# Optimization experiments

Hardware: AMD Instinct MI355X
Metric: run time of the kernel (lower is better)

Reference implementation:

```python
import jax, jax.numpy as jnp
import numpy as np

B, S, D, H, C = 2, 2048, 1024, 16, 64

def setup_inputs() -> dict:
    key = jax.random.key(0)
    kx, kq, kk, kv, ko = jax.random.split(key, 5)
    scale = 0.02
    return {
        "x": jax.random.normal(kx, (B, S, D), dtype=jnp.float32),
        "Wq": jax.random.normal(kq, (D, H, C), dtype=jnp.float32) * scale,
        "Wk": jax.random.normal(kk, (D, H, C), dtype=jnp.float32) * scale,
        "Wv": jax.random.normal(kv, (D, H, C), dtype=jnp.float32) * scale,
        "Wo": jax.random.normal(ko, (H, C, D), dtype=jnp.float32) * scale,
    }

def reference(x, Wq, Wk, Wv, Wo):
    # project to per-head q/k/v: [B,S,H,C]
    q = jnp.einsum('bqd,dhc->bqhc', x, Wq)
    k = jnp.einsum('bkd,dhc->bkhc', x, Wk)
    v = jnp.einsum('bkd,dhc->bkhc', x, Wv)
    q = q * (C ** -0.5)
    alphas = jnp.einsum('bqhc,bkhc->bhqk', q, k)  # [B,H,S,S]
    weights = jax.nn.softmax(alphas, axis=-1)
    out = jnp.einsum('bhqk,bkhc->bqhc', weights, v)
    return jnp.einsum('bqhc,hcd->bqd', out, Wo)
```

## Files before the change

### kernel.cpp

```cpp
#include <hip/hip_runtime.h>
#include <hip/hip_bf16.h>
#include <stdint.h>
#include <stddef.h>

typedef __bf16 bf16;
typedef __bf16 bf16x8 __attribute__((ext_vector_type(8)));
typedef float f32x4 __attribute__((ext_vector_type(4)));

#define DEV __device__ __forceinline__

DEV void async16(const bf16* g, bf16* l) {
    __builtin_amdgcn_global_load_lds(
        (const __attribute__((address_space(1))) void*)g,
        (__attribute__((address_space(3))) void*)l,
        16, 0, 0);
}


__global__ void convert_x(const float* __restrict__ in, bf16* __restrict__ out, int n) {
    int i = (blockIdx.x * blockDim.x + threadIdx.x) * 4;
    if (i >= n) return;
    const float4 v = *(const float4*)(in + i);
    bf16 o4[4] = {(bf16)v.x, (bf16)v.y, (bf16)v.z, (bf16)v.w};
    *(uint2*)(out + i) = *(const uint2*)o4;
}

__global__ void transpose_cvt_all(const float* __restrict__ Wq, const float* __restrict__ Wk,
                                  const float* __restrict__ Wv, const float* __restrict__ Wo,
                                  bf16* __restrict__ WqkvT, bf16* __restrict__ WoT) {
    const float* src;
    bf16* dst;
    float scale = 1.0f;
    switch (blockIdx.z) {
        case 0: src = Wq; dst = WqkvT; scale = 0.125f * 1.4426950408889634f; break;
        case 1: src = Wk; dst = WqkvT + 1024 * 1024; break;
        case 2: src = Wv; dst = WqkvT + 2 * 1024 * 1024; break;
        default: src = Wo; dst = WoT; break;
    }
    __shared__ float t[32][33];
    const int c0 = blockIdx.x * 32, r0 = blockIdx.y * 32;
    const int tx = threadIdx.x & 31, ty = threadIdx.x >> 5;
#pragma unroll
    for (int i = 0; i < 32; i += 8)
        t[ty + i][tx] = src[(size_t)(r0 + ty + i) * 1024 + c0 + tx];
    __syncthreads();
#pragma unroll
    for (int i = 0; i < 32; i += 8)
        dst[(size_t)(c0 + ty + i) * 1024 + r0 + tx] = (bf16)(t[tx][ty + i] * scale);
}

__global__ void transpose_v(const bf16* __restrict__ V, bf16* __restrict__ VT) {
    __shared__ bf16 t[32][33];
    const int c0 = blockIdx.x * 32, r0 = blockIdx.y * 32;
    const int tx = threadIdx.x & 31, ty = threadIdx.x >> 5;
#pragma unroll
    for (int i = 0; i < 32; i += 8)
        t[ty + i][tx] = V[(size_t)(r0 + ty + i) * 3072 + c0 + tx];
    __syncthreads();
#pragma unroll
    for (int i = 0; i < 32; i += 8)
        VT[(size_t)(c0 + ty + i) * 4096 + r0 + tx] = t[tx][ty + i];
}


template <bool OUT_F32>
__global__ __launch_bounds__(256, 3) void gemm_bt(
    const bf16* __restrict__ A, const bf16* __restrict__ BT, void* __restrict__ Cout,
    int M, int N, int K) {
    __shared__ __attribute__((aligned(16))) bf16 As[2 * 128 * 32];
    __shared__ __attribute__((aligned(16))) bf16 Bs[2 * 128 * 32];
    const int tid = threadIdx.x;
    const int wid = tid >> 6;
    const int lane = tid & 63;
    const int quad = lane >> 4;
    const int l16 = lane & 15;
    const int wm = wid >> 1, wn = wid & 1;
    const int m0 = blockIdx.y * 128, n0 = blockIdx.x * 128;

    const int srow = wid * 32 + (lane >> 2);
    const int skcol = (lane & 3) * 8;
    const bf16* ag = A + (size_t)(m0 + srow) * K + skcol;
    const bf16* bg = BT + (size_t)(n0 + srow) * K + skcol;

    f32x4 acc[4][4];
#pragma unroll
    for (int i = 0; i < 4; ++i)
#pragma unroll
        for (int j = 0; j < 4; ++j) acc[i][j] = (f32x4){0.f, 0.f, 0.f, 0.f};

    for (int k0 = 0; k0 < K; k0 += 64) {
#pragma unroll
        for (int p = 0; p < 2; ++p) {
            async16(ag + k0 + p * 32, &As[p * 4096 + (wid * 32) * 32]);
            async16(ag + (size_t)16 * K + k0 + p * 32, &As[p * 4096 + (wid * 32 + 16) * 32]);
            async16(bg + k0 + p * 32, &Bs[p * 4096 + (wid * 32) * 32]);
            async16(bg + (size_t)16 * K + k0 + p * 32, &Bs[p * 4096 + (wid * 32 + 16) * 32]);
        }
        __syncthreads();

#pragma unroll
        for (int ks = 0; ks < 2; ++ks) {
            bf16x8 af[4], bfr[4];
#pragma unroll
            for (int mi = 0; mi < 4; ++mi)
                af[mi] = *(const bf16x8*)&As[ks * 4096 + (wm * 64 + mi * 16 + l16) * 32 + quad * 8];
#pragma unroll
            for (int ni = 0; ni < 4; ++ni)
                bfr[ni] = *(const bf16x8*)&Bs[ks * 4096 + (wn * 64 + ni * 16 + l16) * 32 + quad * 8];
#pragma unroll
            for (int mi = 0; mi < 4; ++mi)
#pragma unroll
                for (int ni = 0; ni < 4; ++ni)
                    acc[mi][ni] = __builtin_amdgcn_mfma_f32_16x16x32_bf16(
                        af[mi], bfr[ni], acc[mi][ni], 0, 0, 0);
        }
        __syncthreads();
    }

    if (OUT_F32) {
        float* C = (float*)Cout;
#pragma unroll
        for (int mi = 0; mi < 4; ++mi)
#pragma unroll
            for (int ni = 0; ni < 4; ++ni)
#pragma unroll
                for (int r = 0; r < 4; ++r)
                    C[(size_t)(m0 + wm * 64 + mi * 16 + quad * 4 + r) * N +
                      (n0 + wn * 64 + ni * 16 + l16)] = acc[mi][ni][r];
    } else {
        bf16* C = (bf16*)Cout;
#pragma unroll
        for (int mi = 0; mi < 4; ++mi)
#pragma unroll
            for (int ni = 0; ni < 4; ++ni)
#pragma unroll
                for (int r = 0; r < 4; ++r)
                    C[(size_t)(m0 + wm * 64 + mi * 16 + quad * 4 + r) * N +
                      (n0 + wn * 64 + ni * 16 + l16)] = (bf16)acc[mi][ni][r];
    }
}


__global__ __launch_bounds__(256, 4) void flash_attn(
    const bf16* __restrict__ QKV, const bf16* __restrict__ VT,
    float* __restrict__ op, float* __restrict__ lp) {
    constexpr int LDK = 72;
    constexpr int LDP = 68;
    __shared__ __attribute__((aligned(16))) bf16 Ks[64 * LDK];
    __shared__ __attribute__((aligned(16))) bf16 Vs[64 * LDK];
    __shared__ __attribute__((aligned(16))) bf16 Ps[128 * LDP];

    const int tid = threadIdx.x, wid = tid >> 6, lane = tid & 63;
    const int quad = lane >> 4, l16 = lane & 15;
    const int qt = blockIdx.x;
    const int bh = blockIdx.y;
    const int kh = blockIdx.z;
    const int b = bh >> 4, h = bh & 15;
    const int q0 = qt * 128;

    const int row8 = tid >> 3, col8 = (tid & 7) * 8;

    {
        const bf16* qg = QKV + (size_t)(b * 2048 + q0 + row8) * 3072 + h * 64 + col8;
#pragma unroll
        for (int p = 0; p < 4; ++p)
            *(bf16x8*)&Ps[(p * 32 + row8) * LDP + col8] =
                *(const bf16x8*)(qg + (size_t)(p * 32) * 3072);
    }
    __syncthreads();
    bf16x8 qf[2][2];
#pragma unroll
    for (int mi = 0; mi < 2; ++mi)
#pragma unroll
        for (int ks = 0; ks < 2; ++ks)
            qf[mi][ks] = *(const bf16x8*)&Ps[(wid * 32 + mi * 16 + l16) * LDP + ks * 32 + quad * 8];

    const bf16* kg = QKV + (size_t)(b * 2048 + kh * 1024 + row8) * 3072 + 1024 + h * 64 + col8;
    const bf16* vg = VT + (size_t)(h * 64 + row8) * 4096 + b * 2048 + kh * 1024 + col8;

    bf16x8 kr0 = *(const bf16x8*)(kg);
    bf16x8 kr1 = *(const bf16x8*)(kg + (size_t)32 * 3072);
    bf16x8 vr0 = *(const bf16x8*)(vg);
    bf16x8 vr1 = *(const bf16x8*)(vg + (size_t)32 * 4096);

    f32x4 o[2][4];
    float lsum[2][4];
#pragma unroll
    for (int mi = 0; mi < 2; ++mi) {
#pragma unroll
        for (int ni = 0; ni < 4; ++ni) o[mi][ni] = (f32x4){0.f, 0.f, 0.f, 0.f};
#pragma unroll
        for (int r = 0; r < 4; ++r) lsum[mi][r] = 0.f;
    }

    for (int kc = 0; kc < 16; ++kc) {
        *(bf16x8*)&Ks[row8 * LDK + col8] = kr0;
        *(bf16x8*)&Ks[(row8 + 32) * LDK + col8] = kr1;
        *(bf16x8*)&Vs[row8 * LDK + col8] = vr0;
        *(bf16x8*)&Vs[(row8 + 32) * LDK + col8] = vr1;
        __syncthreads();

        if (kc < 15) {
            const size_t ko = (size_t)(kc + 1) * 64;
            kr0 = *(const bf16x8*)(kg + ko * 3072);
            kr1 = *(const bf16x8*)(kg + (ko + 32) * 3072);
            vr0 = *(const bf16x8*)(vg + ko);
            vr1 = *(const bf16x8*)(vg + (size_t)32 * 4096 + ko);
        }

        f32x4 s[2][4];
#pragma unroll
        for (int mi = 0; mi < 2; ++mi)
#pragma unroll
            for (int ni = 0; ni < 4; ++ni) s[mi][ni] = (f32x4){0.f, 0.f, 0.f, 0.f};
#pragma unroll
        for (int ni = 0; ni < 4; ++ni) {
            const bf16x8 kf0 = *(const bf16x8*)&Ks[(ni * 16 + l16) * LDK + quad * 8];
            const bf16x8 kf1 = *(const bf16x8*)&Ks[(ni * 16 + l16) * LDK + 32 + quad * 8];
#pragma unroll
            for (int mi = 0; mi < 2; ++mi) {
                s[mi][ni] = __builtin_amdgcn_mfma_f32_16x16x32_bf16(qf[mi][0], kf0, s[mi][ni], 0, 0, 0);
                s[mi][ni] = __builtin_amdgcn_mfma_f32_16x16x32_bf16(qf[mi][1], kf1, s[mi][ni], 0, 0, 0);
            }
        }

#pragma unroll
        for (int mi = 0; mi < 2; ++mi)
#pragma unroll
            for (int ni = 0; ni < 4; ++ni)
#pragma unroll
                for (int r = 0; r < 4; ++r) {
                    const float p = __builtin_amdgcn_exp2f(s[mi][ni][r]);
                    lsum[mi][r] += p;
                    Ps[(wid * 32 + mi * 16 + quad * 4 + r) * LDP + ni * 16 + l16] = (bf16)p;
                }

#pragma unroll
        for (int ks = 0; ks < 2; ++ks) {
            bf16x8 pf[2];
#pragma unroll
            for (int mi = 0; mi < 2; ++mi)
                pf[mi] = *(const bf16x8*)&Ps[(wid * 32 + mi * 16 + l16) * LDP + ks * 32 + quad * 8];
#pragma unroll
            for (int ni = 0; ni < 4; ++ni) {
                const bf16x8 vf = *(const bf16x8*)&Vs[(ni * 16 + l16) * LDK + ks * 32 + quad * 8];
#pragma unroll
                for (int mi = 0; mi < 2; ++mi)
                    o[mi][ni] = __builtin_amdgcn_mfma_f32_16x16x32_bf16(pf[mi], vf, o[mi][ni], 0, 0, 0);
            }
        }
        __syncthreads();
    }

#pragma unroll
    for (int off = 1; off < 16; off <<= 1)
#pragma unroll
        for (int mi = 0; mi < 2; ++mi)
#pragma unroll
            for (int r = 0; r < 4; ++r) lsum[mi][r] += __shfl_xor(lsum[mi][r], off);

    if (l16 == 0) {
#pragma unroll
        for (int mi = 0; mi < 2; ++mi)
#pragma unroll
            for (int r = 0; r < 4; ++r)
                lp[(size_t)kh * 4096 * 16 +
                   (size_t)(b * 2048 + q0 + wid * 32 + mi * 16 + quad * 4 + r) * 16 + h] = lsum[mi][r];
    }
#pragma unroll
    for (int mi = 0; mi < 2; ++mi)
#pragma unroll
        for (int ni = 0; ni < 4; ++ni)
#pragma unroll
            for (int r = 0; r < 4; ++r)
                op[(size_t)kh * 4096 * 1024 +
                   (size_t)(b * 2048 + q0 + wid * 32 + mi * 16 + quad * 4 + r) * 1024 +
                   (h * 64 + ni * 16 + l16)] = o[mi][ni][r];
}

__global__ void combine_att(const float* __restrict__ op, const float* __restrict__ lp,
                            bf16* __restrict__ att) {
    const int idx = (blockIdx.x * 256 + threadIdx.x) * 4;
    const int q = idx >> 10, h = (idx & 1023) >> 6;
    const float4 a = *(const float4*)(op + idx);
    const float4 c = *(const float4*)(op + (size_t)4096 * 1024 + idx);
    const float l = lp[q * 16 + h] + lp[4096 * 16 + q * 16 + h];
    const float inv = 1.0f / l;
    bf16 r[4] = {(bf16)((a.x + c.x) * inv), (bf16)((a.y + c.y) * inv),
                 (bf16)((a.z + c.z) * inv), (bf16)((a.w + c.w) * inv)};
    *(uint2*)(att + idx) = *(const uint2*)r;
}


extern "C" void kernel_launch(void* const* d_in, const int* in_sizes, int n_in,
                              void* d_out, int out_size, void* d_ws, size_t ws_size,
                              hipStream_t stream) {
    (void)in_sizes; (void)n_in; (void)out_size; (void)ws_size;
    const float* x  = (const float*)d_in[0];
    const float* Wq = (const float*)d_in[1];
    const float* Wk = (const float*)d_in[2];
    const float* Wv = (const float*)d_in[3];
    const float* Wo = (const float*)d_in[4];

    char* ws = (char*)d_ws;
    bf16* xb    = (bf16*)(ws);
    bf16* att   = xb;
    bf16* WqkvT = (bf16*)(ws + (size_t)8  * 1024 * 1024);
    bf16* WoT   = (bf16*)(ws + (size_t)14 * 1024 * 1024);
    bf16* QKV   = (bf16*)(ws + (size_t)16 * 1024 * 1024);
    bf16* VT    = (bf16*)(ws + (size_t)40 * 1024 * 1024);
    float* op   = (float*)(ws + (size_t)48 * 1024 * 1024);
    float* lp   = (float*)(ws + (size_t)80 * 1024 * 1024);

    const int n_x = 2 * 2048 * 1024;
    convert_x<<<n_x / (256 * 4), 256, 0, stream>>>(x, xb, n_x);

    transpose_cvt_all<<<dim3(32, 32, 4), 256, 0, stream>>>(Wq, Wk, Wv, Wo, WqkvT, WoT);

    gemm_bt<false><<<dim3(3072 / 128, 4096 / 128), 256, 0, stream>>>(
        xb, WqkvT, QKV, 4096, 3072, 1024);

    transpose_v<<<dim3(32, 128), 256, 0, stream>>>(QKV + 2048, VT);

    flash_attn<<<dim3(16, 32, 2), 256, 0, stream>>>(QKV, VT, op, lp);

    combine_att<<<4096, 256, 0, stream>>>(op, lp, att);

    gemm_bt<true><<<dim3(1024 / 128, 4096 / 128), 256, 0, stream>>>(
        att, WoT, (float*)d_out, 4096, 1024, 1024);
}
```

Baseline: 205.0 us.

## Fuse attention normalization into flash kernel with in-register P and intra-block key split

The flash attention kernel is restructured. It computes S transposed so that the softmax probabilities stay in registers and feed the PV MFMA directly, zero-padding half of the MFMA K dimension. Keys are split across the four waves of a block and the partial outputs are reduced through LDS. This replaces the grid-level key split, the fp32 partial-output and denominator buffers, and the separate combine kernel. K and V are read straight from global memory without LDS staging. The costs are wasted MFMA work from the padding, heavy register pressure (launch bounds lowered to 2), and half as many blocks.

```diff
diff --git a/kernel.cpp b/kernel.cpp
--- a/kernel.cpp
+++ b/kernel.cpp
@@ -4,6 +4,7 @@
 #include <stddef.h>
 
 typedef __bf16 bf16;
+typedef __bf16 bf16x4 __attribute__((ext_vector_type(4)));
 typedef __bf16 bf16x8 __attribute__((ext_vector_type(8)));
 typedef float f32x4 __attribute__((ext_vector_type(4)));
 
@@ -141,154 +142,135 @@
 }
 
 
-__global__ __launch_bounds__(256, 4) void flash_attn(
-    const bf16* __restrict__ QKV, const bf16* __restrict__ VT,
-    float* __restrict__ op, float* __restrict__ lp) {
-    constexpr int LDK = 72;
-    constexpr int LDP = 68;
-    __shared__ __attribute__((aligned(16))) bf16 Ks[64 * LDK];
-    __shared__ __attribute__((aligned(16))) bf16 Vs[64 * LDK];
-    __shared__ __attribute__((aligned(16))) bf16 Ps[128 * LDP];
+__global__ __launch_bounds__(256, 2) void flash_attn(
+    const bf16* __restrict__ QKV, const bf16* __restrict__ VT, bf16* __restrict__ att) {
+    __shared__ float Osc[2][32 * 256];
+    __shared__ float Lred[4][128];
+    __shared__ float Linv[128];
 
     const int tid = threadIdx.x, wid = tid >> 6, lane = tid & 63;
     const int quad = lane >> 4, l16 = lane & 15;
     const int qt = blockIdx.x;
     const int bh = blockIdx.y;
-    const int kh = blockIdx.z;
     const int b = bh >> 4, h = bh & 15;
     const int q0 = qt * 128;
 
-    const int row8 = tid >> 3, col8 = (tid & 7) * 8;
-
+    bf16x8 qf[8][2];
     {
-        const bf16* qg = QKV + (size_t)(b * 2048 + q0 + row8) * 3072 + h * 64 + col8;
-#pragma unroll
-        for (int p = 0; p < 4; ++p)
-            *(bf16x8*)&Ps[(p * 32 + row8) * LDP + col8] =
-                *(const bf16x8*)(qg + (size_t)(p * 32) * 3072);
-    }
-    __syncthreads();
-    bf16x8 qf[2][2];
-#pragma unroll
-    for (int mi = 0; mi < 2; ++mi)
-#pragma unroll
-        for (int ks = 0; ks < 2; ++ks)
-            qf[mi][ks] = *(const bf16x8*)&Ps[(wid * 32 + mi * 16 + l16) * LDP + ks * 32 + quad * 8];
-
-    const bf16* kg = QKV + (size_t)(b * 2048 + kh * 1024 + row8) * 3072 + 1024 + h * 64 + col8;
-    const bf16* vg = VT + (size_t)(h * 64 + row8) * 4096 + b * 2048 + kh * 1024 + col8;
-
-    bf16x8 kr0 = *(const bf16x8*)(kg);
-    bf16x8 kr1 = *(const bf16x8*)(kg + (size_t)32 * 3072);
-    bf16x8 vr0 = *(const bf16x8*)(vg);
-    bf16x8 vr1 = *(const bf16x8*)(vg + (size_t)32 * 4096);
-
-    f32x4 o[2][4];
-    float lsum[2][4];
-#pragma unroll
-    for (int mi = 0; mi < 2; ++mi) {
-#pragma unroll
-        for (int ni = 0; ni < 4; ++ni) o[mi][ni] = (f32x4){0.f, 0.f, 0.f, 0.f};
-#pragma unroll
-        for (int r = 0; r < 4; ++r) lsum[mi][r] = 0.f;
-    }
-
-    for (int kc = 0; kc < 16; ++kc) {
-        *(bf16x8*)&Ks[row8 * LDK + col8] = kr0;
-        *(bf16x8*)&Ks[(row8 + 32) * LDK + col8] = kr1;
-        *(bf16x8*)&Vs[row8 * LDK + col8] = vr0;
-        *(bf16x8*)&Vs[(row8 + 32) * LDK + col8] = vr1;
-        __syncthreads();
-
-        if (kc < 15) {
-            const size_t ko = (size_t)(kc + 1) * 64;
-            kr0 = *(const bf16x8*)(kg + ko * 3072);
-            kr1 = *(const bf16x8*)(kg + (ko + 32) * 3072);
-            vr0 = *(const bf16x8*)(vg + ko);
-            vr1 = *(const bf16x8*)(vg + (size_t)32 * 4096 + ko);
+        const bf16* qbase = QKV + (size_t)(b * 2048 + q0 + l16) * 3072 + h * 64 + quad * 8;
+#pragma unroll
+        for (int mi = 0; mi < 8; ++mi)
+#pragma unroll
+            for (int ks = 0; ks < 2; ++ks)
+                qf[mi][ks] = *(const bf16x8*)(qbase + (size_t)mi * 16 * 3072 + ks * 32);
+    }
+
+    const bf16* kbase = QKV + (size_t)(b * 2048 + wid * 16 + l16) * 3072 + 1024 + h * 64 + quad * 8;
+    const bf16* vbase = VT + (size_t)(h * 64 + l16) * 4096 + b * 2048 + wid * 16 + quad * 4;
+
+    f32x4 o[8][4];
+#pragma unroll
+    for (int mi = 0; mi < 8; ++mi)
+#pragma unroll
+        for (int ct = 0; ct < 4; ++ct) o[mi][ct] = (f32x4){0.f, 0.f, 0.f, 0.f};
+    float lsum[8];
+#pragma unroll
+    for (int mi = 0; mi < 8; ++mi) lsum[mi] = 0.f;
+
+    for (int kc = 0; kc < 32; ++kc) {
+        const bf16* kp = kbase + (size_t)kc * 64 * 3072;
+        const bf16x8 kf0 = *(const bf16x8*)(kp);
+        const bf16x8 kf1 = *(const bf16x8*)(kp + 32);
+
+        const bf16* vp = vbase + kc * 64;
+        bf16x8 vf[4];
+#pragma unroll
+        for (int ct = 0; ct < 4; ++ct) {
+            const bf16x4 t = *(const bf16x4*)(vp + (size_t)ct * 16 * 4096);
+            vf[ct] = (bf16x8){t[0], t[1], t[2], t[3],
+                              (bf16)0.f, (bf16)0.f, (bf16)0.f, (bf16)0.f};
         }
 
-        f32x4 s[2][4];
-#pragma unroll
-        for (int mi = 0; mi < 2; ++mi)
-#pragma unroll
-            for (int ni = 0; ni < 4; ++ni) s[mi][ni] = (f32x4){0.f, 0.f, 0.f, 0.f};
-#pragma unroll
-        for (int ni = 0; ni < 4; ++ni) {
-            const bf16x8 kf0 = *(const bf16x8*)&Ks[(ni * 16 + l16) * LDK + quad * 8];
-            const bf16x8 kf1 = *(const bf16x8*)&Ks[(ni * 16 + l16) * LDK + 32 + quad * 8];
-#pragma unroll
-            for (int mi = 0; mi < 2; ++mi) {
-                s[mi][ni] = __builtin_amdgcn_mfma_f32_16x16x32_bf16(qf[mi][0], kf0, s[mi][ni], 0, 0, 0);
-                s[mi][ni] = __builtin_amdgcn_mfma_f32_16x16x32_bf16(qf[mi][1], kf1, s[mi][ni], 0, 0, 0);
+#pragma unroll
+        for (int mi = 0; mi < 8; ++mi) {
+            f32x4 s = (f32x4){0.f, 0.f, 0.f, 0.f};
+            s = __builtin_amdgcn_mfma_f32_16x16x32_bf16(kf0, qf[mi][0], s, 0, 0, 0);
+            s = __builtin_amdgcn_mfma_f32_16x16x32_bf16(kf1, qf[mi][1], s, 0, 0, 0);
+
+            const float p0 = __builtin_amdgcn_exp2f(s[0]);
+            const float p1 = __builtin_amdgcn_exp2f(s[1]);
+            const float p2 = __builtin_amdgcn_exp2f(s[2]);
+            const float p3 = __builtin_amdgcn_exp2f(s[3]);
+            lsum[mi] += (p0 + p1) + (p2 + p3);
+            const bf16x8 pf = (bf16x8){(bf16)p0, (bf16)p1, (bf16)p2, (bf16)p3,
+                                       (bf16)0.f, (bf16)0.f, (bf16)0.f, (bf16)0.f};
+#pragma unroll
+            for (int ct = 0; ct < 4; ++ct)
+                o[mi][ct] = __builtin_amdgcn_mfma_f32_16x16x32_bf16(pf, vf[ct], o[mi][ct], 0, 0, 0);
+        }
+    }
+
+#pragma unroll
+    for (int mi = 0; mi < 8; ++mi) {
+        lsum[mi] += __shfl_xor(lsum[mi], 16);
+        lsum[mi] += __shfl_xor(lsum[mi], 32);
+    }
+    if (quad == 0) {
+#pragma unroll
+        for (int mi = 0; mi < 8; ++mi) Lred[wid][mi * 16 + l16] = lsum[mi];
+    }
+    if (wid >= 2) {
+        float* dst = &Osc[wid - 2][0];
+#pragma unroll
+        for (int mi = 0; mi < 8; ++mi)
+#pragma unroll
+            for (int ct = 0; ct < 4; ++ct)
+                *(f32x4*)(dst + (mi * 4 + ct) * 256 + lane * 4) = o[mi][ct];
+    }
+    __syncthreads();
+
+    if (tid < 128) {
+        const float l = Lred[0][tid] + Lred[1][tid] + Lred[2][tid] + Lred[3][tid];
+        Linv[tid] = 1.0f / l;
+    }
+    if (wid < 2) {
+        const float* src = &Osc[wid][0];
+#pragma unroll
+        for (int mi = 0; mi < 8; ++mi)
+#pragma unroll
+            for (int ct = 0; ct < 4; ++ct)
+                o[mi][ct] += *(const f32x4*)(src + (mi * 4 + ct) * 256 + lane * 4);
+    }
+    __syncthreads();
+
+    if (wid == 1) {
+        float* dst = &Osc[0][0];
+#pragma unroll
+        for (int mi = 0; mi < 8; ++mi)
+#pragma unroll
+            for (int ct = 0; ct < 4; ++ct)
+                *(f32x4*)(dst + (mi * 4 + ct) * 256 + lane * 4) = o[mi][ct];
+    }
+    __syncthreads();
+
+    if (wid == 0) {
+        const float* src = &Osc[0][0];
+#pragma unroll
+        for (int mi = 0; mi < 8; ++mi)
+#pragma unroll
+            for (int ct = 0; ct < 4; ++ct)
+                o[mi][ct] += *(const f32x4*)(src + (mi * 4 + ct) * 256 + lane * 4);
+#pragma unroll
+        for (int mi = 0; mi < 8; ++mi)
+#pragma unroll
+            for (int r = 0; r < 4; ++r) {
+                const float inv = Linv[mi * 16 + quad * 4 + r];
+                bf16* orow = att + (size_t)(b * 2048 + q0 + mi * 16 + quad * 4 + r) * 1024 + h * 64 + l16;
+#pragma unroll
+                for (int ct = 0; ct < 4; ++ct)
+                    orow[ct * 16] = (bf16)(o[mi][ct][r] * inv);
             }
-        }
-
-#pragma unroll
-        for (int mi = 0; mi < 2; ++mi)
-#pragma unroll
-            for (int ni = 0; ni < 4; ++ni)
-#pragma unroll
-                for (int r = 0; r < 4; ++r) {
-                    const float p = __builtin_amdgcn_exp2f(s[mi][ni][r]);
-                    lsum[mi][r] += p;
-                    Ps[(wid * 32 + mi * 16 + quad * 4 + r) * LDP + ni * 16 + l16] = (bf16)p;
-                }
-
-#pragma unroll
-        for (int ks = 0; ks < 2; ++ks) {
-            bf16x8 pf[2];
-#pragma unroll
-            for (int mi = 0; mi < 2; ++mi)
-                pf[mi] = *(const bf16x8*)&Ps[(wid * 32 + mi * 16 + l16) * LDP + ks * 32 + quad * 8];
-#pragma unroll
-            for (int ni = 0; ni < 4; ++ni) {
-                const bf16x8 vf = *(const bf16x8*)&Vs[(ni * 16 + l16) * LDK + ks * 32 + quad * 8];
-#pragma unroll
-                for (int mi = 0; mi < 2; ++mi)
-                    o[mi][ni] = __builtin_amdgcn_mfma_f32_16x16x32_bf16(pf[mi], vf, o[mi][ni], 0, 0, 0);
-            }
-        }
-        __syncthreads();
-    }
-
-#pragma unroll
-    for (int off = 1; off < 16; off <<= 1)
-#pragma unroll
-        for (int mi = 0; mi < 2; ++mi)
-#pragma unroll
-            for (int r = 0; r < 4; ++r) lsum[mi][r] += __shfl_xor(lsum[mi][r], off);
-
-    if (l16 == 0) {
-#pragma unroll
-        for (int mi = 0; mi < 2; ++mi)
-#pragma unroll
-            for (int r = 0; r < 4; ++r)
-                lp[(size_t)kh * 4096 * 16 +
-                   (size_t)(b * 2048 + q0 + wid * 32 + mi * 16 + quad * 4 + r) * 16 + h] = lsum[mi][r];
-    }
-#pragma unroll
-    for (int mi = 0; mi < 2; ++mi)
-#pragma unroll
-        for (int ni = 0; ni < 4; ++ni)
-#pragma unroll
-            for (int r = 0; r < 4; ++r)
-                op[(size_t)kh * 4096 * 1024 +
-                   (size_t)(b * 2048 + q0 + wid * 32 + mi * 16 + quad * 4 + r) * 1024 +
-                   (h * 64 + ni * 16 + l16)] = o[mi][ni][r];
-}
-
-__global__ void combine_att(const float* __restrict__ op, const float* __restrict__ lp,
-                            bf16* __restrict__ att) {
-    const int idx = (blockIdx.x * 256 + threadIdx.x) * 4;
-    const int q = idx >> 10, h = (idx & 1023) >> 6;
-    const float4 a = *(const float4*)(op + idx);
-    const float4 c = *(const float4*)(op + (size_t)4096 * 1024 + idx);
-    const float l = lp[q * 16 + h] + lp[4096 * 16 + q * 16 + h];
-    const float inv = 1.0f / l;
-    bf16 r[4] = {(bf16)((a.x + c.x) * inv), (bf16)((a.y + c.y) * inv),
-                 (bf16)((a.z + c.z) * inv), (bf16)((a.w + c.w) * inv)};
-    *(uint2*)(att + idx) = *(const uint2*)r;
+    }
 }
 
 
@@ -309,8 +291,6 @@
     bf16* WoT   = (bf16*)(ws + (size_t)14 * 1024 * 1024);
     bf16* QKV   = (bf16*)(ws + (size_t)16 * 1024 * 1024);
     bf16* VT    = (bf16*)(ws + (size_t)40 * 1024 * 1024);
-    float* op   = (float*)(ws + (size_t)48 * 1024 * 1024);
-    float* lp   = (float*)(ws + (size_t)80 * 1024 * 1024);
 
     const int n_x = 2 * 2048 * 1024;
     convert_x<<<n_x / (256 * 4), 256, 0, stream>>>(x, xb, n_x);
@@ -322,9 +302,7 @@
 
     transpose_v<<<dim3(32, 128), 256, 0, stream>>>(QKV + 2048, VT);
 
-    flash_attn<<<dim3(16, 32, 2), 256, 0, stream>>>(QKV, VT, op, lp);
-
-    combine_att<<<4096, 256, 0, stream>>>(op, lp, att);
+    flash_attn<<<dim3(16, 32), 256, 0, stream>>>(QKV, VT, att);
 
     gemm_bt<true><<<dim3(1024 / 128, 4096 / 128), 256, 0, stream>>>(
         att, WoT, (float*)d_out, 4096, 1024, 1024);
```

Result: faster. 199.4 us (-2.8%).
